# Performance work log

Measured on AMD Instinct MI355X. Metric: run time of the kernel, lower is better.

## Reference

```python
import jax, jax.numpy as jnp
import numpy as np

B, S, D, H = 2, 2048, 1024, 16
HD = D // H
EPS = 1e-5


def layer_norm(x, g, b):
    mu = jnp.mean(x, axis=-1, keepdims=True)
    var = jnp.mean(jnp.square(x - mu), axis=-1, keepdims=True)
    return (x - mu) * jax.lax.rsqrt(var + EPS) * g + b


def setup_inputs() -> dict:
    key = jax.random.key(0)
    ks = jax.random.split(key, 10)
    s = 0.02
    return {
        'x': jax.random.normal(ks[0], (B, S, D), jnp.float32),
        'Wq': jax.random.normal(ks[1], (D, D), jnp.float32) * s,
        'bq': jnp.zeros((D,), jnp.float32),
        'Wk': jax.random.normal(ks[2], (D, D), jnp.float32) * s,
        'bk': jnp.zeros((D,), jnp.float32),
        'Wv': jax.random.normal(ks[3], (D, D), jnp.float32) * s,
        'bv': jnp.zeros((D,), jnp.float32),
        'W1': jax.random.normal(ks[4], (D, 4 * D), jnp.float32) * s,
        'b1': jnp.zeros((4 * D,), jnp.float32),
        'W2': jax.random.normal(ks[5], (4 * D, D), jnp.float32) * s,
        'b2': jnp.zeros((D,), jnp.float32),
        'g1': jnp.ones((D,), jnp.float32),
        'be1': jnp.zeros((D,), jnp.float32),
        'g2': jnp.ones((D,), jnp.float32),
        'be2': jnp.zeros((D,), jnp.float32),
    }


def reference(x, Wq, bq, Wk, bk, Wv, bv, W1, b1, W2, b2, g1, be1, g2, be2):
    b, s, d = x.shape
    # QKV projections, split heads: [B,H,S,HD]
    Q = (x @ Wq + bq).reshape(b, s, H, HD).transpose(0, 2, 1, 3)
    K = (x @ Wk + bk).reshape(b, s, H, HD).transpose(0, 2, 1, 3)
    V = (x @ Wv + bv).reshape(b, s, H, HD).transpose(0, 2, 1, 3)
    score = jnp.einsum('bhqd,bhkd->bhqk', Q, K) / jnp.sqrt(jnp.float32(HD))
    attn = jax.nn.softmax(score, axis=-1)
    out = jnp.einsum('bhqk,bhkd->bhqd', attn, V)
    out = out.transpose(0, 2, 1, 3).reshape(b, s, d)
    # dropout(p=0.1) is identity in eval mode
    out = layer_norm(out + x, g1, be1)
    ffn = jax.nn.gelu(out @ W1 + b1, approximate=False) @ W2 + b2
    # NOTE: faithful to source: norm2(output + output), i.e. 2*ffn_out
    return layer_norm(ffn + ffn, g2, be2)
```

## Files before the change

kernel.cpp:

```cpp
#include <hip/hip_runtime.h>
#include <hip/hip_bf16.h>

typedef __hip_bfloat16 bf16;
typedef __attribute__((ext_vector_type(8))) short short8;
typedef __attribute__((ext_vector_type(4))) float floatx4;

struct __align__(8) bf16x4 { bf16 v[4]; };

#define LOG2E 1.4426950408889634f

__device__ __forceinline__ void gload_lds16(const void* g, void* l) {
  __builtin_amdgcn_global_load_lds(
      (const __attribute__((address_space(1))) void*)g,
      (__attribute__((address_space(3))) void*)l, 16, 0, 0);
}

__device__ __forceinline__ floatx4 mfma16(short8 a, short8 b, floatx4 c) {
  return __builtin_amdgcn_mfma_f32_16x16x32_bf16(a, b, c, 0, 0, 0);
}

__global__ __launch_bounds__(256) void convert_x(const float* __restrict__ x,
                                                 bf16* __restrict__ xb) {
  int i = blockIdx.x * 256 + threadIdx.x;
  float4 v = ((const float4*)x)[i];
  bf16x4 o;
  o.v[0] = __float2bfloat16(v.x);
  o.v[1] = __float2bfloat16(v.y);
  o.v[2] = __float2bfloat16(v.z);
  o.v[3] = __float2bfloat16(v.w);
  ((bf16x4*)xb)[i] = o;
}

__device__ __forceinline__ void transpose_tile(const float* __restrict__ W,
                                               bf16* __restrict__ WT,
                                               int K, int N, int n0, int k0,
                                               int tid) {
  __shared__ float t[64][65];
#pragma unroll
  for (int i = 0; i < 4; ++i) {
    int idx = i * 256 + tid;
    int r = idx >> 4;
    int c = (idx & 15) * 4;
    float4 v = *(const float4*)&W[(size_t)(k0 + r) * N + n0 + c];
    t[r][c] = v.x; t[r][c + 1] = v.y; t[r][c + 2] = v.z; t[r][c + 3] = v.w;
  }
  __syncthreads();
#pragma unroll
  for (int i = 0; i < 4; ++i) {
    int idx = i * 256 + tid;
    int r = idx >> 4;
    int c = (idx & 15) * 4;
    bf16x4 o;
    o.v[0] = __float2bfloat16(t[c][r]);
    o.v[1] = __float2bfloat16(t[c + 1][r]);
    o.v[2] = __float2bfloat16(t[c + 2][r]);
    o.v[3] = __float2bfloat16(t[c + 3][r]);
    *(bf16x4*)&WT[(size_t)(n0 + r) * K + k0 + c] = o;
  }
}

__global__ __launch_bounds__(256) void transpose_w(const float* __restrict__ W,
                                                   bf16* __restrict__ WT,
                                                   int K, int N) {
  transpose_tile(W, WT, K, N, blockIdx.x * 64, blockIdx.y * 64, threadIdx.x);
}

__global__ __launch_bounds__(256) void transpose_qkv(const float* __restrict__ Wq,
                                                     const float* __restrict__ Wk,
                                                     const float* __restrict__ Wv,
                                                     bf16* __restrict__ WT) {
  const float* W = (blockIdx.z == 0) ? Wq : (blockIdx.z == 1) ? Wk : Wv;
  bf16* dst = WT + (size_t)blockIdx.z * 1024 * 1024;
  transpose_tile(W, dst, 1024, 1024, blockIdx.x * 64, blockIdx.y * 64, threadIdx.x);
}

__global__ __launch_bounds__(256) void transpose_v(const bf16* __restrict__ V,
                                                   bf16* __restrict__ Vt) {
  __shared__ bf16 t[64][72];
  const int bh = blockIdx.y;
  const int s0 = blockIdx.x * 64;
  const bf16* src = V + (size_t)bh * 2048 * 64;
  bf16* dst = Vt + (size_t)bh * 64 * 2048;
  const int tid = threadIdx.x;
#pragma unroll
  for (int i = 0; i < 16; ++i) {
    int idx = i * 256 + tid;
    int r = idx >> 6, c = idx & 63;
    t[r][c] = src[(size_t)(s0 + r) * 64 + c];
  }
  __syncthreads();
#pragma unroll
  for (int i = 0; i < 4; ++i) {
    int idx = i * 256 + tid;
    int r = idx >> 4;
    int c = (idx & 15) * 4;
    bf16x4 o;
    o.v[0] = t[r][c]; o.v[1] = t[r][c + 1]; o.v[2] = t[r][c + 2]; o.v[3] = t[r][c + 3];
    dst[(size_t)c * 2048 + s0 + r] = o.v[0];
    dst[(size_t)(c + 1) * 2048 + s0 + r] = o.v[1];
    dst[(size_t)(c + 2) * 2048 + s0 + r] = o.v[2];
    dst[(size_t)(c + 3) * 2048 + s0 + r] = o.v[3];
  }
}

template <int MODE>
__global__ __launch_bounds__(256, 2) void gemm_bt(
    const bf16* __restrict__ A, const bf16* __restrict__ BT,
    const float* __restrict__ bias0, const float* __restrict__ bias1,
    const float* __restrict__ bias2, void* __restrict__ C0,
    void* __restrict__ C1, void* __restrict__ C2,
    int M, int N, int K, int lda, int ldb) {
  __shared__ bf16 As[2][128 * 64];
  __shared__ bf16 Bs[2][128 * 64];
  const int tid = threadIdx.x;
  const int wid = tid >> 6, lane = tid & 63;
  const int l16 = lane & 15, lhi = lane >> 4;
  const int nwg = gridDim.x * gridDim.y;
  const int orig = blockIdx.y * gridDim.x + blockIdx.x;
  const int wflat = (orig & 7) * (nwg >> 3) + (orig >> 3);
  const int bx = wflat % gridDim.x, by = wflat / gridDim.x;
  const int brow = by * 128, bcol = bx * 128;
  const int z = blockIdx.z;
  const size_t koff = (size_t)z * (size_t)K;
  const int wr = (wid >> 1) * 64, wc = (wid & 1) * 64;
  const int swz = (l16 & 7) << 4;
  floatx4 acc[4][4] = {};

  auto stage = [&](int buf, int kt) {
#pragma unroll
    for (int i = 0; i < 4; ++i) {
      const int f = i * 256 + tid;
      const int row = f >> 3;
      const int cb = ((f & 7) * 16) ^ ((row & 7) << 4);
      gload_lds16((const char*)A + ((size_t)(brow + row) * lda + koff + kt) * 2 + cb,
                  (char*)&As[buf][0] + (size_t)f * 16);
      gload_lds16((const char*)BT + ((size_t)(bcol + row) * ldb + koff + kt) * 2 + cb,
                  (char*)&Bs[buf][0] + (size_t)f * 16);
    }
  };

  const int nk = K >> 6;
  stage(0, 0);
  int cur = 0;
  for (int t = 0; t < nk; ++t) {
    if (t + 1 < nk) {
      stage(cur ^ 1, (t + 1) << 6);
      asm volatile("s_waitcnt vmcnt(8)" ::: "memory");
    } else {
      asm volatile("s_waitcnt vmcnt(0)" ::: "memory");
    }
    asm volatile("s_barrier" ::: "memory");
#pragma unroll
    for (int kk = 0; kk < 2; ++kk) {
      short8 af[4], bfr[4];
#pragma unroll
      for (int m = 0; m < 4; ++m)
        af[m] = *(const short8*)((const char*)&As[cur][0] +
                                 (wr + m * 16 + l16) * 128 + ((kk * 64 + lhi * 16) ^ swz));
#pragma unroll
      for (int n = 0; n < 4; ++n)
        bfr[n] = *(const short8*)((const char*)&Bs[cur][0] +
                                  (wc + n * 16 + l16) * 128 + ((kk * 64 + lhi * 16) ^ swz));
      __builtin_amdgcn_s_setprio(1);
#pragma unroll
      for (int m = 0; m < 4; ++m)
#pragma unroll
        for (int n = 0; n < 4; ++n) acc[m][n] = mfma16(af[m], bfr[n], acc[m][n]);
      __builtin_amdgcn_s_setprio(0);
    }
    asm volatile("s_barrier" ::: "memory");
    cur ^= 1;
  }

#pragma unroll
  for (int m = 0; m < 4; ++m) {
    const int rowb = brow + wr + m * 16 + lhi * 4;
#pragma unroll
    for (int n = 0; n < 4; ++n) {
      const int col = bcol + wc + n * 16 + l16;
#pragma unroll
      for (int r = 0; r < 4; ++r) {
        float v = acc[m][n][r];
        const int gr = rowb + r;
        if constexpr (MODE == 0) {
          const int which = col >> 10;
          const int nl = col & 1023;
          const float* bp = (which == 0) ? bias0 : (which == 1) ? bias1 : bias2;
          v += bp[nl];
          const int b = gr >> 11, s = gr & 2047;
          const int h = nl >> 6, hd = nl & 63;
          const size_t dst = ((size_t)(b * 16 + h) * 2048 + s) * 64 + hd;
          bf16* out = (which == 0) ? (bf16*)C0 : (which == 1) ? (bf16*)C1 : (bf16*)C2;
          out[dst] = __float2bfloat16(v);
        } else {
          float* dst = (z == 0) ? (float*)C0 : (float*)C1;
          dst[(size_t)gr * N + col] = v;
        }
      }
    }
  }
}

template <int MODE>
__global__ __launch_bounds__(512, 2) void gemm256(
    const bf16* __restrict__ A, const bf16* __restrict__ BT,
    const float* __restrict__ bias0, void* __restrict__ C0,
    int M, int N, int K, int lda, int ldb) {
  __shared__ bf16 As[2][256 * 64];
  __shared__ bf16 Bs[2][256 * 64];
  const int tid = threadIdx.x;
  const int lane = tid & 63, wid = tid >> 6;
  const int l16 = lane & 15, lhi = lane >> 4;
  const int wm = wid >> 2, wn = wid & 3;
  const int nwg = gridDim.x * gridDim.y;
  const int orig = blockIdx.y * gridDim.x + blockIdx.x;
  const int wflat = (orig & 7) * (nwg >> 3) + (orig >> 3);
  const int bx = wflat % gridDim.x, by = wflat / gridDim.x;
  const int brow = by * 256, bcol = bx * 256;
  const int swz = (l16 & 7) << 4;
  floatx4 acc[8][4] = {};

  auto stage = [&](int buf, int kt) {
#pragma unroll
    for (int i = 0; i < 4; ++i) {
      const int f = i * 512 + tid;
      const int row = f >> 3;
      const int cb = ((f & 7) * 16) ^ ((row & 7) << 4);
      gload_lds16((const char*)A + ((size_t)(brow + row) * lda + kt) * 2 + cb,
                  (char*)&As[buf][0] + (size_t)f * 16);
    }
#pragma unroll
    for (int i = 0; i < 4; ++i) {
      const int f = i * 512 + tid;
      const int row = f >> 3;
      const int cb = ((f & 7) * 16) ^ ((row & 7) << 4);
      gload_lds16((const char*)BT + ((size_t)(bcol + row) * ldb + kt) * 2 + cb,
                  (char*)&Bs[buf][0] + (size_t)f * 16);
    }
  };

  const int nk = K >> 6;
  stage(0, 0);
  asm volatile("s_waitcnt vmcnt(0)" ::: "memory");
  asm volatile("s_barrier" ::: "memory");
  int cur = 0;
  for (int t = 0; t < nk; ++t) {
    const char* Ab = (const char*)&As[cur][0];
    const char* Bb = (const char*)&Bs[cur][0];
    short8 af[8], b0, b1;
#pragma unroll
    for (int m = 0; m < 8; ++m)
      af[m] = *(const short8*)(Ab + (wm * 128 + m * 16 + l16) * 128 + ((lhi * 16) ^ swz));
    b0 = *(const short8*)(Bb + (wn * 64 + l16) * 128 + ((lhi * 16) ^ swz));
    b1 = *(const short8*)(Bb + (wn * 64 + 16 + l16) * 128 + ((lhi * 16) ^ swz));
    if (t + 1 < nk) stage(cur ^ 1, (t + 1) << 6);
    asm volatile("s_barrier" ::: "memory");
    __builtin_amdgcn_s_setprio(1);
#pragma unroll
    for (int m = 0; m < 8; ++m) {
      acc[m][0] = mfma16(af[m], b0, acc[m][0]);
      acc[m][1] = mfma16(af[m], b1, acc[m][1]);
    }
    __builtin_amdgcn_s_setprio(0);
    asm volatile("s_barrier" ::: "memory");
    b0 = *(const short8*)(Bb + (wn * 64 + 32 + l16) * 128 + ((lhi * 16) ^ swz));
    b1 = *(const short8*)(Bb + (wn * 64 + 48 + l16) * 128 + ((lhi * 16) ^ swz));
    asm volatile("s_barrier" ::: "memory");
    __builtin_amdgcn_s_setprio(1);
#pragma unroll
    for (int m = 0; m < 8; ++m) {
      acc[m][2] = mfma16(af[m], b0, acc[m][2]);
      acc[m][3] = mfma16(af[m], b1, acc[m][3]);
    }
    __builtin_amdgcn_s_setprio(0);
    asm volatile("s_barrier" ::: "memory");
#pragma unroll
    for (int m = 0; m < 8; ++m)
      af[m] = *(const short8*)(Ab + (wm * 128 + m * 16 + l16) * 128 + ((64 + lhi * 16) ^ swz));
    b0 = *(const short8*)(Bb + (wn * 64 + l16) * 128 + ((64 + lhi * 16) ^ swz));
    b1 = *(const short8*)(Bb + (wn * 64 + 16 + l16) * 128 + ((64 + lhi * 16) ^ swz));
    asm volatile("s_barrier" ::: "memory");
    __builtin_amdgcn_s_setprio(1);
#pragma unroll
    for (int m = 0; m < 8; ++m) {
      acc[m][0] = mfma16(af[m], b0, acc[m][0]);
      acc[m][1] = mfma16(af[m], b1, acc[m][1]);
    }
    __builtin_amdgcn_s_setprio(0);
    asm volatile("s_barrier" ::: "memory");
    b0 = *(const short8*)(Bb + (wn * 64 + 32 + l16) * 128 + ((64 + lhi * 16) ^ swz));
    b1 = *(const short8*)(Bb + (wn * 64 + 48 + l16) * 128 + ((64 + lhi * 16) ^ swz));
    asm volatile("s_waitcnt vmcnt(0)" ::: "memory");
    asm volatile("s_barrier" ::: "memory");
    __builtin_amdgcn_s_setprio(1);
#pragma unroll
    for (int m = 0; m < 8; ++m) {
      acc[m][2] = mfma16(af[m], b0, acc[m][2]);
      acc[m][3] = mfma16(af[m], b1, acc[m][3]);
    }
    __builtin_amdgcn_s_setprio(0);
    asm volatile("s_barrier" ::: "memory");
    cur ^= 1;
  }

#pragma unroll
  for (int m = 0; m < 8; ++m) {
    const int rowb = brow + wm * 128 + m * 16 + lhi * 4;
#pragma unroll
    for (int n = 0; n < 4; ++n) {
      const int col = bcol + wn * 64 + n * 16 + l16;
#pragma unroll
      for (int r = 0; r < 4; ++r) {
        float v = acc[m][n][r] + bias0[col];
        float gch = 0.5f * v * (1.0f + erff(v * 0.70710678118654752f));
        ((bf16*)C0)[(size_t)(rowb + r) * N + col] = __float2bfloat16(gch);
      }
    }
  }
}

__global__ __launch_bounds__(512, 2) void flash_attn(const bf16* __restrict__ Q,
                                                     const bf16* __restrict__ Kb,
                                                     const bf16* __restrict__ Vt,
                                                     bf16* __restrict__ attn) {
  __shared__ bf16 Ks[2][64 * 64];
  __shared__ bf16 Vs[2][64 * 64];
  __shared__ bf16 Ps[8][16 * 64];
  const int tid = threadIdx.x, wid = tid >> 6, lane = tid & 63;
  const int l16 = lane & 15, lhi = lane >> 4, lhi4 = (lane >> 4) * 4;
  const int bid = blockIdx.x;
  const int w = (bid & 7) * 64 + (bid >> 3);
  const int bh = w >> 4, qtile = w & 15;
  const bf16* Qbh = Q + (size_t)bh * 2048 * 64;
  const char* Kbh = (const char*)(Kb + (size_t)bh * 2048 * 64);
  const char* Vbh = (const char*)(Vt + (size_t)bh * 64 * 2048);
  bf16* Pw = &Ps[wid][0];
  const int q0 = qtile * 128 + wid * 16;
  const int swA = (l16 & 7) << 3;
  const int swzB = (l16 & 7) << 4;

  const int strow = tid >> 3;
  const int stcol = ((tid & 7) * 16) ^ ((strow & 7) << 4);

  short8 qf[2];
#pragma unroll
  for (int kk = 0; kk < 2; ++kk)
    qf[kk] = *(const short8*)&Qbh[(size_t)(q0 + l16) * 64 + kk * 32 + lhi * 8];

  floatx4 o[4] = {};
  float mrow = -1e30f;
  float lrow = 0.0f;
  const float SC = 0.125f * LOG2E;

  auto stage = [&](bf16* Kd, bf16* Vd, int t) {
    const int kvr = t * 64;
    gload_lds16(Kbh + (size_t)(kvr + strow) * 128 + stcol, (char*)Kd + tid * 16);
    gload_lds16(Vbh + (size_t)strow * 4096 + (size_t)kvr * 2 + stcol, (char*)Vd + tid * 16);
  };

  auto tile = [&](bf16* Kc, bf16* Vc, bf16* Kn, bf16* Vn, int t) {
    if (t + 1 < 32) {
      stage(Kn, Vn, t + 1);
      asm volatile("s_waitcnt vmcnt(2)" ::: "memory");
    } else {
      asm volatile("s_waitcnt vmcnt(0)" ::: "memory");
    }
    asm volatile("s_barrier" ::: "memory");

    short8 kf[2][4];
#pragma unroll
    for (int kk = 0; kk < 2; ++kk)
#pragma unroll
      for (int fc = 0; fc < 4; ++fc)
        kf[kk][fc] = *(const short8*)((const char*)Kc + (fc * 16 + l16) * 128 +
                                      ((kk * 64 + lhi * 16) ^ swzB));

    floatx4 sf[4] = {};
    __builtin_amdgcn_s_setprio(1);
#pragma unroll
    for (int kk = 0; kk < 2; ++kk)
#pragma unroll
      for (int fc = 0; fc < 4; ++fc) sf[fc] = mfma16(kf[kk][fc], qf[kk], sf[fc]);
    __builtin_amdgcn_s_setprio(0);

    {
      float a0 = fmaxf(fmaxf(sf[0][0], sf[0][1]), fmaxf(sf[0][2], sf[0][3]));
      float a1 = fmaxf(fmaxf(sf[1][0], sf[1][1]), fmaxf(sf[1][2], sf[1][3]));
      float a2 = fmaxf(fmaxf(sf[2][0], sf[2][1]), fmaxf(sf[2][2], sf[2][3]));
      float a3 = fmaxf(fmaxf(sf[3][0], sf[3][1]), fmaxf(sf[3][2], sf[3][3]));
      float mx = fmaxf(fmaxf(a0, a1), fmaxf(a2, a3));
      mx = fmaxf(mx, __shfl_xor(mx, 16));
      mx = fmaxf(mx, __shfl_xor(mx, 32));
      mx *= SC;
      if (__any(mx > mrow + 11.54f)) {
        const float mnew = fmaxf(mrow, mx);
        const float corr = exp2f(mrow - mnew);
        mrow = mnew;
        lrow *= corr;
#pragma unroll
        for (int r = 0; r < 4; ++r) {
          const float c = __shfl(corr, lhi4 + r);
#pragma unroll
          for (int fc = 0; fc < 4; ++fc) o[fc][r] *= c;
        }
      }
      const float m = mrow;
#pragma unroll
      for (int fc = 0; fc < 4; ++fc)
#pragma unroll
        for (int r = 0; r < 4; ++r) {
          const float p = exp2f(fmaf(sf[fc][r], SC, -m));
          sf[fc][r] = p;
          lrow += p;
        }
#pragma unroll
      for (int fc = 0; fc < 4; ++fc) {
        bf16x4 pk;
#pragma unroll
        for (int r = 0; r < 4; ++r) pk.v[r] = __float2bfloat16(sf[fc][r]);
        *(bf16x4*)&Pw[l16 * 64 + ((fc * 16 + lhi4) ^ swA)] = pk;
      }
    }

    short8 pf[2];
#pragma unroll
    for (int kk = 0; kk < 2; ++kk)
      pf[kk] = *(const short8*)&Pw[l16 * 64 + ((kk * 32 + lhi * 8) ^ swA)];
    __builtin_amdgcn_s_setprio(1);
#pragma unroll
    for (int kk = 0; kk < 2; ++kk) {
      short8 vf[4];
#pragma unroll
      for (int fc = 0; fc < 4; ++fc)
        vf[fc] = *(const short8*)((const char*)Vc + (fc * 16 + l16) * 128 +
                                  ((kk * 64 + lhi * 16) ^ swzB));
#pragma unroll
      for (int fc = 0; fc < 4; ++fc) o[fc] = mfma16(pf[kk], vf[fc], o[fc]);
    }
    __builtin_amdgcn_s_setprio(0);

    asm volatile("s_barrier" ::: "memory");
  };

  stage(&Ks[0][0], &Vs[0][0], 0);
  for (int t = 0; t < 32; t += 2) {
    tile(&Ks[0][0], &Vs[0][0], &Ks[1][0], &Vs[1][0], t);
    tile(&Ks[1][0], &Vs[1][0], &Ks[0][0], &Vs[0][0], t + 1);
  }

  lrow += __shfl_xor(lrow, 16);
  lrow += __shfl_xor(lrow, 32);

  const int b = bh >> 4, h = bh & 15;
#pragma unroll
  for (int r = 0; r < 4; ++r) {
    const float lr = __shfl(lrow, lhi4 + r);
    const float inv = 1.0f / lr;
    const int s = q0 + lhi4 + r;
    const size_t rowbase = (size_t)(b * 2048 + s) * 1024 + h * 64;
#pragma unroll
    for (int fc = 0; fc < 4; ++fc)
      attn[rowbase + fc * 16 + l16] = __float2bfloat16(o[fc][r] * inv);
  }
}

__global__ __launch_bounds__(256) void ln_res(const bf16* __restrict__ attn,
                                              const bf16* __restrict__ xb,
                                              const float* __restrict__ g,
                                              const float* __restrict__ be,
                                              bf16* __restrict__ out) {
  __shared__ float sa[4], sb[4];
  const int row = blockIdx.x;
  const size_t base = (size_t)row * 1024;
  const int tid = threadIdx.x;
  const int c0 = tid * 4;
  bf16x4 xv = *(const bf16x4*)(xb + base + c0);
  bf16x4 av = *(const bf16x4*)(attn + base + c0);
  float v[4];
  v[0] = __bfloat162float(xv.v[0]) + __bfloat162float(av.v[0]);
  v[1] = __bfloat162float(xv.v[1]) + __bfloat162float(av.v[1]);
  v[2] = __bfloat162float(xv.v[2]) + __bfloat162float(av.v[2]);
  v[3] = __bfloat162float(xv.v[3]) + __bfloat162float(av.v[3]);
  float s = v[0] + v[1] + v[2] + v[3];
  float ss = v[0]*v[0] + v[1]*v[1] + v[2]*v[2] + v[3]*v[3];
#pragma unroll
  for (int d = 32; d > 0; d >>= 1) { s += __shfl_down(s, d); ss += __shfl_down(ss, d); }
  const int wid = tid >> 6, lane = tid & 63;
  if (lane == 0) { sa[wid] = s; sb[wid] = ss; }
  __syncthreads();
  if (tid == 0) { sa[0] = sa[0]+sa[1]+sa[2]+sa[3]; sb[0] = sb[0]+sb[1]+sb[2]+sb[3]; }
  __syncthreads();
  s = sa[0]; ss = sb[0];
  const float mu = s * (1.0f / 1024.0f);
  const float var = ss * (1.0f / 1024.0f) - mu * mu;
  const float rs = rsqrtf(var + 1e-5f);
  float4 gv = *(const float4*)(g + c0);
  float4 bv = *(const float4*)(be + c0);
  bf16x4 o;
  o.v[0] = __float2bfloat16((v[0]-mu)*rs*gv.x + bv.x);
  o.v[1] = __float2bfloat16((v[1]-mu)*rs*gv.y + bv.y);
  o.v[2] = __float2bfloat16((v[2]-mu)*rs*gv.z + bv.z);
  o.v[3] = __float2bfloat16((v[3]-mu)*rs*gv.w + bv.w);
  *(bf16x4*)(out + base + c0) = o;
}

__global__ __launch_bounds__(256) void ln2_kernel(const float* __restrict__ y0,
                                                  const float* __restrict__ y1,
                                                  const float* __restrict__ b2,
                                                  const float* __restrict__ g,
                                                  const float* __restrict__ be,
                                                  float* __restrict__ out) {
  __shared__ float sa[4], sb[4];
  const int row = blockIdx.x;
  const size_t base = (size_t)row * 1024;
  const int tid = threadIdx.x;
  const int c0 = tid * 4;
  float4 ya = *(const float4*)(y0 + base + c0);
  float4 yb = *(const float4*)(y1 + base + c0);
  float4 bb = *(const float4*)(b2 + c0);
  float v[4] = {2.0f * (ya.x + yb.x + bb.x), 2.0f * (ya.y + yb.y + bb.y),
                2.0f * (ya.z + yb.z + bb.z), 2.0f * (ya.w + yb.w + bb.w)};
  float s = v[0] + v[1] + v[2] + v[3];
  float ss = v[0]*v[0] + v[1]*v[1] + v[2]*v[2] + v[3]*v[3];
#pragma unroll
  for (int d = 32; d > 0; d >>= 1) { s += __shfl_down(s, d); ss += __shfl_down(ss, d); }
  const int wid = tid >> 6, lane = tid & 63;
  if (lane == 0) { sa[wid] = s; sb[wid] = ss; }
  __syncthreads();
  if (tid == 0) { sa[0] = sa[0]+sa[1]+sa[2]+sa[3]; sb[0] = sb[0]+sb[1]+sb[2]+sb[3]; }
  __syncthreads();
  s = sa[0]; ss = sb[0];
  const float mu = s * (1.0f / 1024.0f);
  const float var = ss * (1.0f / 1024.0f) - mu * mu;
  const float rs = rsqrtf(var + 1e-5f);
  float4 gv = *(const float4*)(g + c0);
  float4 bv = *(const float4*)(be + c0);
  float4 o;
  o.x = (v[0]-mu)*rs*gv.x + bv.x;
  o.y = (v[1]-mu)*rs*gv.y + bv.y;
  o.z = (v[2]-mu)*rs*gv.z + bv.z;
  o.w = (v[3]-mu)*rs*gv.w + bv.w;
  *(float4*)(out + base + c0) = o;
}

extern "C" void kernel_launch(void* const* d_in, const int* in_sizes, int n_in,
                              void* d_out, int out_size, void* d_ws, size_t ws_size,
                              hipStream_t stream) {
  const float* x   = (const float*)d_in[0];
  const float* Wq  = (const float*)d_in[1];
  const float* bq  = (const float*)d_in[2];
  const float* Wk  = (const float*)d_in[3];
  const float* bk  = (const float*)d_in[4];
  const float* Wv  = (const float*)d_in[5];
  const float* bv  = (const float*)d_in[6];
  const float* W1  = (const float*)d_in[7];
  const float* b1  = (const float*)d_in[8];
  const float* W2  = (const float*)d_in[9];
  const float* b2  = (const float*)d_in[10];
  const float* g1  = (const float*)d_in[11];
  const float* be1 = (const float*)d_in[12];
  const float* g2  = (const float*)d_in[13];
  const float* be2 = (const float*)d_in[14];

  char* ws = (char*)d_ws;
  bf16* xb    = (bf16*)(ws + 0ull);
  bf16* WqkvT = (bf16*)(ws + 8388608ull);
  bf16* W1T   = (bf16*)(ws + 14680064ull);
  bf16* W2T   = (bf16*)(ws + 23068672ull);
  bf16* Qb    = (bf16*)(ws + 31457280ull);
  bf16* Kb    = (bf16*)(ws + 39845888ull);
  bf16* Vb    = (bf16*)(ws + 48234496ull);
  bf16* Vt    = (bf16*)(ws + 56623104ull);
  bf16* h1    = (bf16*)(ws + 31457280ull);
  bf16* attn  = (bf16*)(ws + 65011712ull);
  bf16* ln1   = (bf16*)(ws + 73400320ull);
  float* y2a  = (float*)(ws + 0ull);
  float* y2b  = (float*)(ws + 65011712ull);
  float* out  = (float*)d_out;

  convert_x<<<4096, 256, 0, stream>>>(x, xb);
  transpose_qkv<<<dim3(16, 16, 3), 256, 0, stream>>>(Wq, Wk, Wv, WqkvT);
  transpose_w<<<dim3(64, 16), 256, 0, stream>>>(W1, W1T, 1024, 4096);
  transpose_w<<<dim3(16, 64), 256, 0, stream>>>(W2, W2T, 4096, 1024);

  gemm_bt<0><<<dim3(24, 32), 256, 0, stream>>>(xb, WqkvT, bq, bk, bv,
                                               (void*)Qb, (void*)Kb, (void*)Vb,
                                               4096, 3072, 1024, 1024, 1024);
  transpose_v<<<dim3(32, 32), 256, 0, stream>>>(Vb, Vt);
  flash_attn<<<512, 512, 0, stream>>>(Qb, Kb, Vt, attn);
  ln_res<<<4096, 256, 0, stream>>>(attn, xb, g1, be1, ln1);
  gemm256<1><<<dim3(16, 16), 512, 0, stream>>>(ln1, W1T, b1, (void*)h1,
                                               4096, 4096, 1024, 1024, 1024);
  gemm_bt<3><<<dim3(8, 32, 2), 256, 0, stream>>>(h1, W2T, nullptr, nullptr, nullptr,
                                                 (void*)y2a, (void*)y2b, nullptr,
                                                 4096, 1024, 2048, 4096, 4096);
  ln2_kernel<<<4096, 256, 0, stream>>>(y2a, y2b, b2, g2, be2, out);
}
```

Before: 244.3 us.

## Merge prep kernels, store FFN2 partials as bf16, hoist V loads, coalesce V transpose

The input conversion and the three weight transposes become a single launch split by block index, which removes launch overhead and lets the pieces run concurrently. The split-K partial outputs of the second FFN GEMM are now written and read as bf16 instead of fp32, halving that traffic at some cost in precision. In flash attention, the V fragment loads are issued before the softmax so their latency overlaps with it, at the cost of extra registers. The V transpose now writes coalesced scalar stores.

```diff
diff --git a/kernel.cpp b/kernel.cpp
--- a/kernel.cpp
+++ b/kernel.cpp
@@ -17,18 +17,6 @@
 
 __device__ __forceinline__ floatx4 mfma16(short8 a, short8 b, floatx4 c) {
   return __builtin_amdgcn_mfma_f32_16x16x32_bf16(a, b, c, 0, 0, 0);
-}
-
-__global__ __launch_bounds__(256) void convert_x(const float* __restrict__ x,
-                                                 bf16* __restrict__ xb) {
-  int i = blockIdx.x * 256 + threadIdx.x;
-  float4 v = ((const float4*)x)[i];
-  bf16x4 o;
-  o.v[0] = __float2bfloat16(v.x);
-  o.v[1] = __float2bfloat16(v.y);
-  o.v[2] = __float2bfloat16(v.z);
-  o.v[3] = __float2bfloat16(v.w);
-  ((bf16x4*)xb)[i] = o;
 }
 
 __device__ __forceinline__ void transpose_tile(const float* __restrict__ W,
@@ -59,19 +47,39 @@
   }
 }
 
-__global__ __launch_bounds__(256) void transpose_w(const float* __restrict__ W,
-                                                   bf16* __restrict__ WT,
-                                                   int K, int N) {
-  transpose_tile(W, WT, K, N, blockIdx.x * 64, blockIdx.y * 64, threadIdx.x);
-}
-
-__global__ __launch_bounds__(256) void transpose_qkv(const float* __restrict__ Wq,
-                                                     const float* __restrict__ Wk,
-                                                     const float* __restrict__ Wv,
-                                                     bf16* __restrict__ WT) {
-  const float* W = (blockIdx.z == 0) ? Wq : (blockIdx.z == 1) ? Wk : Wv;
-  bf16* dst = WT + (size_t)blockIdx.z * 1024 * 1024;
-  transpose_tile(W, dst, 1024, 1024, blockIdx.x * 64, blockIdx.y * 64, threadIdx.x);
+__global__ __launch_bounds__(256) void prep(const float* __restrict__ x,
+                                            bf16* __restrict__ xb,
+                                            const float* __restrict__ Wq,
+                                            const float* __restrict__ Wk,
+                                            const float* __restrict__ Wv,
+                                            bf16* __restrict__ WqkvT,
+                                            const float* __restrict__ W1,
+                                            bf16* __restrict__ W1T,
+                                            const float* __restrict__ W2,
+                                            bf16* __restrict__ W2T) {
+  const int bid = blockIdx.x, tid = threadIdx.x;
+  if (bid < 4096) {
+    int i = bid * 256 + tid;
+    float4 v = ((const float4*)x)[i];
+    bf16x4 o;
+    o.v[0] = __float2bfloat16(v.x);
+    o.v[1] = __float2bfloat16(v.y);
+    o.v[2] = __float2bfloat16(v.z);
+    o.v[3] = __float2bfloat16(v.w);
+    ((bf16x4*)xb)[i] = o;
+  } else if (bid < 4864) {
+    const int idx = bid - 4096;
+    const int z = idx >> 8, t = idx & 255;
+    const float* W = (z == 0) ? Wq : (z == 1) ? Wk : Wv;
+    transpose_tile(W, WqkvT + (size_t)z * 1024 * 1024, 1024, 1024,
+                   (t & 15) * 64, (t >> 4) * 64, tid);
+  } else if (bid < 5888) {
+    const int idx = bid - 4864;
+    transpose_tile(W1, W1T, 1024, 4096, (idx & 63) * 64, (idx >> 6) * 64, tid);
+  } else {
+    const int idx = bid - 5888;
+    transpose_tile(W2, W2T, 4096, 1024, (idx & 15) * 64, (idx >> 4) * 64, tid);
+  }
 }
 
 __global__ __launch_bounds__(256) void transpose_v(const bf16* __restrict__ V,
@@ -90,16 +98,10 @@
   }
   __syncthreads();
 #pragma unroll
-  for (int i = 0; i < 4; ++i) {
+  for (int i = 0; i < 16; ++i) {
     int idx = i * 256 + tid;
-    int r = idx >> 4;
-    int c = (idx & 15) * 4;
-    bf16x4 o;
-    o.v[0] = t[r][c]; o.v[1] = t[r][c + 1]; o.v[2] = t[r][c + 2]; o.v[3] = t[r][c + 3];
-    dst[(size_t)c * 2048 + s0 + r] = o.v[0];
-    dst[(size_t)(c + 1) * 2048 + s0 + r] = o.v[1];
-    dst[(size_t)(c + 2) * 2048 + s0 + r] = o.v[2];
-    dst[(size_t)(c + 3) * 2048 + s0 + r] = o.v[3];
+    int r = idx >> 6, c = idx & 63;
+    dst[(size_t)r * 2048 + s0 + c] = t[c][r];
   }
 }
 
@@ -193,15 +195,14 @@
           bf16* out = (which == 0) ? (bf16*)C0 : (which == 1) ? (bf16*)C1 : (bf16*)C2;
           out[dst] = __float2bfloat16(v);
         } else {
-          float* dst = (z == 0) ? (float*)C0 : (float*)C1;
-          dst[(size_t)gr * N + col] = v;
+          bf16* dst = (z == 0) ? (bf16*)C0 : (bf16*)C1;
+          dst[(size_t)gr * N + col] = __float2bfloat16(v);
         }
       }
     }
   }
 }
 
-template <int MODE>
 __global__ __launch_bounds__(512, 2) void gemm256(
     const bf16* __restrict__ A, const bf16* __restrict__ BT,
     const float* __restrict__ bias0, void* __restrict__ C0,
@@ -383,6 +384,14 @@
       for (int fc = 0; fc < 4; ++fc) sf[fc] = mfma16(kf[kk][fc], qf[kk], sf[fc]);
     __builtin_amdgcn_s_setprio(0);
 
+    short8 vf[2][4];
+#pragma unroll
+    for (int kk = 0; kk < 2; ++kk)
+#pragma unroll
+      for (int fc = 0; fc < 4; ++fc)
+        vf[kk][fc] = *(const short8*)((const char*)Vc + (fc * 16 + l16) * 128 +
+                                      ((kk * 64 + lhi * 16) ^ swzB));
+
     {
       float a0 = fmaxf(fmaxf(sf[0][0], sf[0][1]), fmaxf(sf[0][2], sf[0][3]));
       float a1 = fmaxf(fmaxf(sf[1][0], sf[1][1]), fmaxf(sf[1][2], sf[1][3]));
@@ -428,15 +437,9 @@
       pf[kk] = *(const short8*)&Pw[l16 * 64 + ((kk * 32 + lhi * 8) ^ swA)];
     __builtin_amdgcn_s_setprio(1);
 #pragma unroll
-    for (int kk = 0; kk < 2; ++kk) {
-      short8 vf[4];
-#pragma unroll
-      for (int fc = 0; fc < 4; ++fc)
-        vf[fc] = *(const short8*)((const char*)Vc + (fc * 16 + l16) * 128 +
-                                  ((kk * 64 + lhi * 16) ^ swzB));
-#pragma unroll
-      for (int fc = 0; fc < 4; ++fc) o[fc] = mfma16(pf[kk], vf[fc], o[fc]);
-    }
+    for (int kk = 0; kk < 2; ++kk)
+#pragma unroll
+      for (int fc = 0; fc < 4; ++fc) o[fc] = mfma16(pf[kk], vf[kk][fc], o[fc]);
     __builtin_amdgcn_s_setprio(0);
 
     asm volatile("s_barrier" ::: "memory");
@@ -504,8 +507,8 @@
   *(bf16x4*)(out + base + c0) = o;
 }
 
-__global__ __launch_bounds__(256) void ln2_kernel(const float* __restrict__ y0,
-                                                  const float* __restrict__ y1,
+__global__ __launch_bounds__(256) void ln2_kernel(const bf16* __restrict__ y0,
+                                                  const bf16* __restrict__ y1,
                                                   const float* __restrict__ b2,
                                                   const float* __restrict__ g,
                                                   const float* __restrict__ be,
@@ -515,11 +518,14 @@
   const size_t base = (size_t)row * 1024;
   const int tid = threadIdx.x;
   const int c0 = tid * 4;
-  float4 ya = *(const float4*)(y0 + base + c0);
-  float4 yb = *(const float4*)(y1 + base + c0);
+  bf16x4 ya = *(const bf16x4*)(y0 + base + c0);
+  bf16x4 yb = *(const bf16x4*)(y1 + base + c0);
   float4 bb = *(const float4*)(b2 + c0);
-  float v[4] = {2.0f * (ya.x + yb.x + bb.x), 2.0f * (ya.y + yb.y + bb.y),
-                2.0f * (ya.z + yb.z + bb.z), 2.0f * (ya.w + yb.w + bb.w)};
+  float v[4];
+  v[0] = 2.0f * (__bfloat162float(ya.v[0]) + __bfloat162float(yb.v[0]) + bb.x);
+  v[1] = 2.0f * (__bfloat162float(ya.v[1]) + __bfloat162float(yb.v[1]) + bb.y);
+  v[2] = 2.0f * (__bfloat162float(ya.v[2]) + __bfloat162float(yb.v[2]) + bb.z);
+  v[3] = 2.0f * (__bfloat162float(ya.v[3]) + __bfloat162float(yb.v[3]) + bb.w);
   float s = v[0] + v[1] + v[2] + v[3];
   float ss = v[0]*v[0] + v[1]*v[1] + v[2]*v[2] + v[3]*v[3];
 #pragma unroll
@@ -574,14 +580,11 @@
   bf16* h1    = (bf16*)(ws + 31457280ull);
   bf16* attn  = (bf16*)(ws + 65011712ull);
   bf16* ln1   = (bf16*)(ws + 73400320ull);
-  float* y2a  = (float*)(ws + 0ull);
-  float* y2b  = (float*)(ws + 65011712ull);
+  bf16* y2a   = (bf16*)(ws + 0ull);
+  bf16* y2b   = (bf16*)(ws + 65011712ull);
   float* out  = (float*)d_out;
 
-  convert_x<<<4096, 256, 0, stream>>>(x, xb);
-  transpose_qkv<<<dim3(16, 16, 3), 256, 0, stream>>>(Wq, Wk, Wv, WqkvT);
-  transpose_w<<<dim3(64, 16), 256, 0, stream>>>(W1, W1T, 1024, 4096);
-  transpose_w<<<dim3(16, 64), 256, 0, stream>>>(W2, W2T, 4096, 1024);
+  prep<<<6912, 256, 0, stream>>>(x, xb, Wq, Wk, Wv, WqkvT, W1, W1T, W2, W2T);
 
   gemm_bt<0><<<dim3(24, 32), 256, 0, stream>>>(xb, WqkvT, bq, bk, bv,
                                                (void*)Qb, (void*)Kb, (void*)Vb,
@@ -589,8 +592,8 @@
   transpose_v<<<dim3(32, 32), 256, 0, stream>>>(Vb, Vt);
   flash_attn<<<512, 512, 0, stream>>>(Qb, Kb, Vt, attn);
   ln_res<<<4096, 256, 0, stream>>>(attn, xb, g1, be1, ln1);
-  gemm256<1><<<dim3(16, 16), 512, 0, stream>>>(ln1, W1T, b1, (void*)h1,
-                                               4096, 4096, 1024, 1024, 1024);
+  gemm256<<<dim3(16, 16), 512, 0, stream>>>(ln1, W1T, b1, (void*)h1,
+                                            4096, 4096, 1024, 1024, 1024);
   gemm_bt<3><<<dim3(8, 32, 2), 256, 0, stream>>>(h1, W2T, nullptr, nullptr, nullptr,
                                                  (void*)y2a, (void*)y2b, nullptr,
                                                  4096, 1024, 2048, 4096, 4096);
```

Measured after the change: 231.1 us. 5.4% less time.
